# Kernel tuning notes

Measured on AMD Instinct MI355X. Metric: run time of the kernel, lower is better.

Reference implementation:

```python
import jax, jax.numpy as jnp
import numpy as np

IN_DIM = 768
N_HEADS = 12
HEAD_DIM = IN_DIM // N_HEADS


def setup_inputs() -> dict:
    key = jax.random.key(0)
    k1, k2, k3, k4, k5 = jax.random.split(key, 5)
    x = jax.random.normal(k1, (2, 2048, IN_DIM), dtype=jnp.float32)
    s = 1.0 / np.sqrt(IN_DIM)
    W_qkv = jax.random.uniform(k2, (IN_DIM, 3 * IN_DIM), jnp.float32, -s, s)
    b_qkv = jax.random.uniform(k3, (3 * IN_DIM,), jnp.float32, -s, s)
    W_out = jax.random.uniform(k4, (IN_DIM, IN_DIM), jnp.float32, -s, s)
    b_out = jax.random.uniform(k5, (IN_DIM,), jnp.float32, -s, s)
    return {"x": x, "W_qkv": W_qkv, "b_qkv": b_qkv, "W_out": W_out, "b_out": b_out}


def reference(x, W_qkv, b_qkv, W_out, b_out):
    B, N, D = x.shape
    qkv = x @ W_qkv + b_qkv  # [B, N, 3D]
    qkv = qkv.reshape(B, N, 3, N_HEADS, HEAD_DIM)
    qkv = jnp.transpose(qkv, (2, 0, 3, 1, 4))  # [3, B, H, N, Dh]
    q, k, v = qkv[0], qkv[1], qkv[2]
    scale = 1.0 / np.sqrt(HEAD_DIM)
    scores = jnp.einsum("bhqd,bhkd->bhqk", q, k) * scale  # [B, H, N, N]
    attn = jax.nn.softmax(scores, axis=-1)
    out = jnp.einsum("bhqk,bhkd->bhqd", attn, v)  # [B, H, N, Dh]
    out = jnp.transpose(out, (0, 2, 1, 3)).reshape(B, N, D)
    return out @ W_out + b_out
```

## Files before the change

kernel.cpp:

```cpp
#include <hip/hip_runtime.h>

#define DEVI __device__ __forceinline__

typedef __attribute__((ext_vector_type(8))) short short8;
typedef __attribute__((ext_vector_type(4))) float f32x4;
typedef __attribute__((ext_vector_type(16))) float f32x16;

DEVI unsigned short f32_to_bf16(float f) {
  unsigned int u = __float_as_uint(f);
  u += 0x7fffu + ((u >> 16) & 1u);
  return (unsigned short)(u >> 16);
}
DEVI float bf16_to_f32(unsigned short h) {
  return __uint_as_float(((unsigned int)h) << 16);
}

DEVI void gld_lds16(const void* g, void* l) {
  __builtin_amdgcn_global_load_lds(
      (__attribute__((address_space(1))) void*)(g),
      (__attribute__((address_space(3))) void*)(l), 16, 0, 0);
}

__global__ void k_cast_bf16(const float* __restrict__ in, unsigned short* __restrict__ out,
                            int total8) {
  int i = blockIdx.x * blockDim.x + threadIdx.x;
  if (i >= total8) return;
  const float* src = in + i * 8;
  short8 v;
#pragma unroll
  for (int j = 0; j < 8; ++j) v[j] = (short)f32_to_bf16(src[j]);
  *(short8*)&out[(size_t)i * 8] = v;
}

__global__ __launch_bounds__(256) void k_cast_Bt(const float* __restrict__ W,
                                                 unsigned short* __restrict__ Wt,
                                                 int K, int N) {
  int kt = blockIdx.x, nt = blockIdx.y;
  __shared__ float t[32][33];
  int tid = threadIdx.x;
#pragma unroll
  for (int p = 0; p < 4; ++p) {
    int idx = tid + p * 256;
    int rr = idx >> 5, cc = idx & 31;
    t[rr][cc] = W[(size_t)(kt * 32 + rr) * N + nt * 32 + cc];
  }
  __syncthreads();
#pragma unroll
  for (int p = 0; p < 4; ++p) {
    int idx = tid + p * 256;
    int rn = idx >> 5, ck = idx & 31;
    Wt[(size_t)(nt * 32 + rn) * K + kt * 32 + ck] = f32_to_bf16(t[ck][rn]);
  }
}

__global__ __launch_bounds__(256) void k_gemm_qkv(const unsigned short* __restrict__ A,
                                                  const unsigned short* __restrict__ Bt,
                                                  const float* __restrict__ bias,
                                                  int M, int N, int K,
                                                  unsigned short* __restrict__ Qo,
                                                  unsigned short* __restrict__ Ko,
                                                  unsigned short* __restrict__ Vo) {
  __shared__ __align__(16) unsigned short As[128 * 32];
  __shared__ __align__(16) unsigned short Bs[128 * 32];
  int tid = threadIdx.x;
  int tm = blockIdx.x, tn = blockIdx.y;
  int lane = tid & 63, wid = tid >> 6;
  int wr = wid >> 1, wc = wid & 1;
  int g = lane >> 4, lr = lane & 15;
  f32x4 acc[4][4] = {};
  int srow = tid >> 2;
  int scol = (tid & 3) * 8;
  const unsigned short* Ab = A + (size_t)tm * 128 * K;
  const unsigned short* Bb = Bt + (size_t)tn * 128 * K;
  for (int k0 = 0; k0 < K; k0 += 32) {
    gld_lds16(Ab + (size_t)srow * K + k0 + scol, &As[srow * 32 + scol]);
    gld_lds16(Ab + (size_t)(srow + 64) * K + k0 + scol, &As[(srow + 64) * 32 + scol]);
    gld_lds16(Bb + (size_t)srow * K + k0 + scol, &Bs[srow * 32 + scol]);
    gld_lds16(Bb + (size_t)(srow + 64) * K + k0 + scol, &Bs[(srow + 64) * 32 + scol]);
    __syncthreads();
    short8 a[4], b[4];
#pragma unroll
    for (int m = 0; m < 4; ++m)
      a[m] = *(const short8*)&As[(wr * 64 + m * 16 + lr) * 32 + g * 8];
#pragma unroll
    for (int n = 0; n < 4; ++n)
      b[n] = *(const short8*)&Bs[(wc * 64 + n * 16 + lr) * 32 + g * 8];
#pragma unroll
    for (int m = 0; m < 4; ++m)
#pragma unroll
      for (int n = 0; n < 4; ++n)
        acc[m][n] = __builtin_amdgcn_mfma_f32_16x16x32_bf16(a[m], b[n], acc[m][n], 0, 0, 0);
    __syncthreads();
  }
  const float QSCALE = 0.125f * 1.4426950408889634f;
#pragma unroll
  for (int m = 0; m < 4; ++m) {
#pragma unroll
    for (int n = 0; n < 4; ++n) {
      int col = tn * 128 + wc * 64 + n * 16 + lr;
      float bv = bias[col];
      int sec = (col >= 1536) ? 2 : ((col >= 768) ? 1 : 0);
      int c = col - sec * 768;
      int hh = c >> 6, d = c & 63;
#pragma unroll
      for (int j = 0; j < 4; ++j) {
        int row = tm * 128 + wr * 64 + m * 16 + g * 4 + j;
        int bb = row >> 11, nn = row & 2047;
        size_t dst = (((size_t)(bb * 12 + hh) << 11) + nn) * 64 + d;
        float outv = acc[m][n][j] + bv;
        if (sec == 0) {
          Qo[dst] = f32_to_bf16(outv * QSCALE);
        } else if (sec == 1) {
          Ko[dst] = f32_to_bf16(outv);
        } else {
          Vo[dst] = f32_to_bf16(outv);
        }
      }
    }
  }
}

__global__ __launch_bounds__(256) void k_gemm2(const unsigned short* __restrict__ A,
                                               const unsigned short* __restrict__ Bt,
                                               const float* __restrict__ bias,
                                               float* __restrict__ C,
                                               int M, int N, int K) {
  __shared__ __align__(16) unsigned short As[64 * 32];
  __shared__ __align__(16) unsigned short Bs[64 * 32];
  int tid = threadIdx.x;
  int tm = blockIdx.x, tn = blockIdx.y;
  int lane = tid & 63, wid = tid >> 6;
  int wr = wid >> 1, wc = wid & 1;
  int g = lane >> 4, lr = lane & 15;
  f32x4 acc[2][2] = {};
  int srow = tid >> 2;
  int scol = (tid & 3) * 8;
  const unsigned short* Ab = A + (size_t)tm * 64 * K;
  const unsigned short* Bb = Bt + (size_t)tn * 64 * K;
  for (int k0 = 0; k0 < K; k0 += 32) {
    gld_lds16(Ab + (size_t)srow * K + k0 + scol, &As[srow * 32 + scol]);
    gld_lds16(Bb + (size_t)srow * K + k0 + scol, &Bs[srow * 32 + scol]);
    __syncthreads();
    short8 a[2], b[2];
#pragma unroll
    for (int m = 0; m < 2; ++m)
      a[m] = *(const short8*)&As[(wr * 32 + m * 16 + lr) * 32 + g * 8];
#pragma unroll
    for (int n = 0; n < 2; ++n)
      b[n] = *(const short8*)&Bs[(wc * 32 + n * 16 + lr) * 32 + g * 8];
#pragma unroll
    for (int m = 0; m < 2; ++m)
#pragma unroll
      for (int n = 0; n < 2; ++n)
        acc[m][n] = __builtin_amdgcn_mfma_f32_16x16x32_bf16(a[m], b[n], acc[m][n], 0, 0, 0);
    __syncthreads();
  }
#pragma unroll
  for (int m = 0; m < 2; ++m) {
#pragma unroll
    for (int n = 0; n < 2; ++n) {
      int col = tn * 64 + wc * 32 + n * 16 + lr;
      float bv = bias[col];
#pragma unroll
      for (int j = 0; j < 4; ++j) {
        int row = tm * 64 + wr * 32 + m * 16 + g * 4 + j;
        C[(size_t)row * N + col] = acc[m][n][j] + bv;
      }
    }
  }
}

__global__ __launch_bounds__(256) void k_v_transpose(const unsigned short* __restrict__ Vc,
                                                     unsigned short* __restrict__ Vt) {
  int bh = blockIdx.x;
  int nt = blockIdx.y;
  __shared__ unsigned short s[64][65];
  int tid = threadIdx.x;
  int r = tid >> 2;
#pragma unroll
  for (int p = 0; p < 2; ++p) {
    int c = (tid & 3) + p * 4;
    short8 v = *(const short8*)&Vc[((size_t)(bh * 2048 + nt * 64 + r)) * 64 + c * 8];
#pragma unroll
    for (int ii = 0; ii < 8; ++ii) s[r][c * 8 + ii] = (unsigned short)v[ii];
  }
  __syncthreads();
  int d = tid >> 2;
#pragma unroll
  for (int p = 0; p < 2; ++p) {
    int c = (tid & 3) + p * 4;
    short8 w;
#pragma unroll
    for (int ii = 0; ii < 8; ++ii) w[ii] = (short)s[c * 8 + ii][d];
    *(short8*)&Vt[((size_t)bh * 64 + d) * 2048 + nt * 64 + c * 8] = w;
  }
}


#define ATTN_STAGE(KSB, VSB, T)                                                          \
  {                                                                                      \
    int kv0 = (T) * 64;                                                                  \
    _Pragma("unroll") for (int it = 0; it < 4; ++it) {                                   \
      int L = tid + it * 128;                                                            \
      int rw = L >> 3, s7 = L & 7;                                                       \
      gld_lds16(Kb + (size_t)(khead + kv0 + rw) * 64 + ((s7 ^ (rw & 7)) * 8),            \
                &KSB[L * 8]);                                                            \
      gld_lds16(Vt + (size_t)(vhead + rw) * 2048 + kv0 + ((s7 ^ (rw & 7)) * 8),          \
                &VSB[L * 8]);                                                            \
    }                                                                                    \
  }

#define BUILD_PA(S, KS0)                                                                 \
  {                                                                                      \
    unsigned int b0, a0, e0, c0;                                                         \
    asm("v_cvt_pk_bf16_f32 %0, %1, %2" : "=v"(b0) : "v"(S[0]), "v"(S[1]));               \
    asm("v_cvt_pk_bf16_f32 %0, %1, %2" : "=v"(a0) : "v"(S[4]), "v"(S[5]));               \
    asm("v_permlane32_swap_b32 %0, %1" : "+v"(b0), "+v"(a0));                            \
    asm("v_cvt_pk_bf16_f32 %0, %1, %2" : "=v"(e0) : "v"(S[2]), "v"(S[3]));               \
    asm("v_cvt_pk_bf16_f32 %0, %1, %2" : "=v"(c0) : "v"(S[6]), "v"(S[7]));               \
    asm("v_permlane32_swap_b32 %0, %1" : "+v"(e0), "+v"(c0));                            \
    paw[KS0][0] = b0; paw[KS0][1] = e0; paw[KS0][2] = a0; paw[KS0][3] = c0;              \
    unsigned int b1, a1, e1, c1;                                                         \
    asm("v_cvt_pk_bf16_f32 %0, %1, %2" : "=v"(b1) : "v"(S[8]), "v"(S[9]));               \
    asm("v_cvt_pk_bf16_f32 %0, %1, %2" : "=v"(a1) : "v"(S[12]), "v"(S[13]));             \
    asm("v_permlane32_swap_b32 %0, %1" : "+v"(b1), "+v"(a1));                            \
    asm("v_cvt_pk_bf16_f32 %0, %1, %2" : "=v"(e1) : "v"(S[10]), "v"(S[11]));             \
    asm("v_cvt_pk_bf16_f32 %0, %1, %2" : "=v"(c1) : "v"(S[14]), "v"(S[15]));             \
    asm("v_permlane32_swap_b32 %0, %1" : "+v"(e1), "+v"(c1));                            \
    paw[KS0 + 1][0] = b1; paw[KS0 + 1][1] = e1; paw[KS0 + 1][2] = a1; paw[KS0 + 1][3] = c1; \
  }

#define PROC_TILE(KSB, VSB)                                                              \
  {                                                                                      \
    f32x16 sa = {}, sb = {};                                                             \
    __builtin_amdgcn_s_setprio(1);                                                       \
    _Pragma("unroll") for (int ds = 0; ds < 4; ++ds) {                                   \
      short8 kf0 = *(const short8*)&KSB[ln31 * 64 + (((ds * 2 + hi) ^ ln7) * 8)];        \
      short8 kf1 = *(const short8*)&KSB[(32 + ln31) * 64 + (((ds * 2 + hi) ^ ln7) * 8)]; \
      sa = __builtin_amdgcn_mfma_f32_32x32x16_bf16(kf0, qf[ds], sa, 0, 0, 0);            \
      sb = __builtin_amdgcn_mfma_f32_32x32x16_bf16(kf1, qf[ds], sb, 0, 0, 0);            \
    }                                                                                    \
    __builtin_amdgcn_s_setprio(0);                                                       \
    _Pragma("unroll") for (int i = 0; i < 16; ++i) {                                     \
      float pv = exp2f(sa[i]);                                                           \
      sa[i] = pv;                                                                        \
      lrun += pv;                                                                        \
    }                                                                                    \
    _Pragma("unroll") for (int i = 0; i < 16; ++i) {                                     \
      float pv = exp2f(sb[i]);                                                           \
      sb[i] = pv;                                                                        \
      lrun += pv;                                                                        \
    }                                                                                    \
    unsigned int paw[4][4];                                                              \
    BUILD_PA(sa, 0)                                                                      \
    BUILD_PA(sb, 2)                                                                      \
    __builtin_amdgcn_s_setprio(1);                                                       \
    _Pragma("unroll") for (int ks = 0; ks < 4; ++ks) {                                   \
      union {                                                                            \
        unsigned int u[4];                                                               \
        short8 s8;                                                                       \
      } pu;                                                                              \
      pu.u[0] = paw[ks][0];                                                              \
      pu.u[1] = paw[ks][1];                                                              \
      pu.u[2] = paw[ks][2];                                                              \
      pu.u[3] = paw[ks][3];                                                              \
      short8 vb0 = *(const short8*)&VSB[ln31 * 64 + (((ks * 2 + hi) ^ ln7) * 8)];        \
      short8 vb1 = *(const short8*)&VSB[(32 + ln31) * 64 + (((ks * 2 + hi) ^ ln7) * 8)]; \
      oacc0 = __builtin_amdgcn_mfma_f32_32x32x16_bf16(pu.s8, vb0, oacc0, 0, 0, 0);       \
      oacc1 = __builtin_amdgcn_mfma_f32_32x32x16_bf16(pu.s8, vb1, oacc1, 0, 0, 0);       \
    }                                                                                    \
    __builtin_amdgcn_s_setprio(0);                                                       \
  }

__global__ __launch_bounds__(128, 3) void k_attn(const unsigned short* __restrict__ Qb,
                                                 const unsigned short* __restrict__ Kb,
                                                 const unsigned short* __restrict__ Vt,
                                                 unsigned short* __restrict__ Xh) {
  int bh = blockIdx.x;
  int qb = blockIdx.y;
  int b = bh / 12, h = bh - b * 12;
  __shared__ __align__(16) unsigned short Ks0[64 * 64], Ks1[64 * 64];
  __shared__ __align__(16) unsigned short Vs0[64 * 64], Vs1[64 * 64];
  int tid = threadIdx.x;
  int wid = tid >> 6, lane = tid & 63;
  int ln31 = lane & 31, hi = lane >> 5, ln7 = lane & 7;
  int khead = bh * 2048;
  int vhead = bh * 64;
  int q0 = qb * 64 + wid * 32;

  short8 qf[4];
#pragma unroll
  for (int ds = 0; ds < 4; ++ds)
    qf[ds] = *(const short8*)&Qb[(size_t)(khead + q0 + ln31) * 64 + ds * 16 + hi * 8];

  float lrun = 0.f;
  f32x16 oacc0 = {}, oacc1 = {};

  ATTN_STAGE(Ks0, Vs0, 0);
  __syncthreads();
#pragma unroll 1
  for (int tt = 0; tt < 16; ++tt) {
    ATTN_STAGE(Ks1, Vs1, 2 * tt + 1);
    PROC_TILE(Ks0, Vs0);
    __syncthreads();
    if (tt < 15) ATTN_STAGE(Ks0, Vs0, 2 * tt + 2);
    PROC_TILE(Ks1, Vs1);
    __syncthreads();
  }

  lrun += __shfl_xor(lrun, 32, 64);
  float linv = 1.0f / lrun;
#pragma unroll
  for (int r = 0; r < 16; ++r) {
    int qrow = (r & 3) + 8 * (r >> 2) + 4 * hi;
    float lf = __shfl(linv, qrow, 64);
    int grow = b * 2048 + q0 + qrow;
    int colb = h * 64 + ln31;
    Xh[(size_t)grow * 768 + colb] = f32_to_bf16(oacc0[r] * lf);
    Xh[(size_t)grow * 768 + colb + 32] = f32_to_bf16(oacc1[r] * lf);
  }
}

extern "C" void kernel_launch(void* const* d_in, const int* in_sizes, int n_in,
                              void* d_out, int out_size, void* d_ws, size_t ws_size,
                              hipStream_t stream) {
  const float* x = (const float*)d_in[0];
  const float* W_qkv = (const float*)d_in[1];
  const float* b_qkv = (const float*)d_in[2];
  const float* W_out = (const float*)d_in[3];
  const float* b_out = (const float*)d_in[4];
  float* out = (float*)d_out;
  char* ws = (char*)d_ws;

  unsigned short* Xh = (unsigned short*)(ws + 0);
  unsigned short* Xb = (unsigned short*)(ws + 18874368);
  unsigned short* Wq_t = (unsigned short*)(ws + 25165824);
  unsigned short* Wo_t = (unsigned short*)(ws + 28704768);
  unsigned short* Qb = (unsigned short*)(ws + 32243712);
  unsigned short* Kb = (unsigned short*)(ws + 38535168);
  unsigned short* Vc = (unsigned short*)(ws + 44826624);
  unsigned short* Vt = (unsigned short*)(ws + 51118080);

  k_cast_bf16<<<(4096 * 768 / 8 + 255) / 256, 256, 0, stream>>>(x, Xb, 4096 * 768 / 8);
  k_cast_Bt<<<dim3(24, 72), 256, 0, stream>>>(W_qkv, Wq_t, 768, 2304);
  k_cast_Bt<<<dim3(24, 24), 256, 0, stream>>>(W_out, Wo_t, 768, 768);
  k_gemm_qkv<<<dim3(32, 18), 256, 0, stream>>>(Xb, Wq_t, b_qkv, 4096, 2304, 768, Qb, Kb, Vc);
  k_v_transpose<<<dim3(24, 32), 256, 0, stream>>>(Vc, Vt);
  k_attn<<<dim3(24, 32), 128, 0, stream>>>(Qb, Kb, Vt, Xh);
  k_gemm2<<<dim3(64, 12), 256, 0, stream>>>(Xh, Wo_t, b_out, out, 4096, 768, 768);
}
```

Before: 118.2 us.

## Split KV tiles across wave pairs in attention with LDS reduction

Attention blocks grow from 2 to 4 waves. Each pair of waves shares one 32-row query slice and splits every 64-key tile into two 32-key halves. At the end the partial outputs and row sums are reduced through LDS before normalising. The aim is more waves per tile and smaller per-wave register use, to raise occupancy and latency hiding. The cost is an extra LDS round trip and a barrier at the end, and each wave does fewer MFMAs per loaded tile.

```diff
diff --git a/kernel.cpp b/kernel.cpp
--- a/kernel.cpp
+++ b/kernel.cpp
@@ -200,8 +200,8 @@
 #define ATTN_STAGE(KSB, VSB, T)                                                          \
   {                                                                                      \
     int kv0 = (T) * 64;                                                                  \
-    _Pragma("unroll") for (int it = 0; it < 4; ++it) {                                   \
-      int L = tid + it * 128;                                                            \
+    _Pragma("unroll") for (int it = 0; it < 2; ++it) {                                   \
+      int L = tid + it * 256;                                                            \
       int rw = L >> 3, s7 = L & 7;                                                       \
       gld_lds16(Kb + (size_t)(khead + kv0 + rw) * 64 + ((s7 ^ (rw & 7)) * 8),            \
                 &KSB[L * 8]);                                                            \
@@ -210,7 +210,7 @@
     }                                                                                    \
   }
 
-#define BUILD_PA(S, KS0)                                                                 \
+#define BUILD_PA(S)                                                                      \
   {                                                                                      \
     unsigned int b0, a0, e0, c0;                                                         \
     asm("v_cvt_pk_bf16_f32 %0, %1, %2" : "=v"(b0) : "v"(S[0]), "v"(S[1]));               \
@@ -219,7 +219,7 @@
     asm("v_cvt_pk_bf16_f32 %0, %1, %2" : "=v"(e0) : "v"(S[2]), "v"(S[3]));               \
     asm("v_cvt_pk_bf16_f32 %0, %1, %2" : "=v"(c0) : "v"(S[6]), "v"(S[7]));               \
     asm("v_permlane32_swap_b32 %0, %1" : "+v"(e0), "+v"(c0));                            \
-    paw[KS0][0] = b0; paw[KS0][1] = e0; paw[KS0][2] = a0; paw[KS0][3] = c0;              \
+    paw[0][0] = b0; paw[0][1] = e0; paw[0][2] = a0; paw[0][3] = c0;                      \
     unsigned int b1, a1, e1, c1;                                                         \
     asm("v_cvt_pk_bf16_f32 %0, %1, %2" : "=v"(b1) : "v"(S[8]), "v"(S[9]));               \
     asm("v_cvt_pk_bf16_f32 %0, %1, %2" : "=v"(a1) : "v"(S[12]), "v"(S[13]));             \
@@ -227,18 +227,16 @@
     asm("v_cvt_pk_bf16_f32 %0, %1, %2" : "=v"(e1) : "v"(S[10]), "v"(S[11]));             \
     asm("v_cvt_pk_bf16_f32 %0, %1, %2" : "=v"(c1) : "v"(S[14]), "v"(S[15]));             \
     asm("v_permlane32_swap_b32 %0, %1" : "+v"(e1), "+v"(c1));                            \
-    paw[KS0 + 1][0] = b1; paw[KS0 + 1][1] = e1; paw[KS0 + 1][2] = a1; paw[KS0 + 1][3] = c1; \
+    paw[1][0] = b1; paw[1][1] = e1; paw[1][2] = a1; paw[1][3] = c1;                      \
   }
 
 #define PROC_TILE(KSB, VSB)                                                              \
   {                                                                                      \
-    f32x16 sa = {}, sb = {};                                                             \
+    f32x16 sa = {};                                                                      \
     __builtin_amdgcn_s_setprio(1);                                                       \
     _Pragma("unroll") for (int ds = 0; ds < 4; ++ds) {                                   \
-      short8 kf0 = *(const short8*)&KSB[ln31 * 64 + (((ds * 2 + hi) ^ ln7) * 8)];        \
-      short8 kf1 = *(const short8*)&KSB[(32 + ln31) * 64 + (((ds * 2 + hi) ^ ln7) * 8)]; \
-      sa = __builtin_amdgcn_mfma_f32_32x32x16_bf16(kf0, qf[ds], sa, 0, 0, 0);            \
-      sb = __builtin_amdgcn_mfma_f32_32x32x16_bf16(kf1, qf[ds], sb, 0, 0, 0);            \
+      short8 kf = *(const short8*)&KSB[(kh * 32 + ln31) * 64 + (((ds * 2 + hi) ^ ln7) * 8)]; \
+      sa = __builtin_amdgcn_mfma_f32_32x32x16_bf16(kf, qf[ds], sa, 0, 0, 0);             \
     }                                                                                    \
     __builtin_amdgcn_s_setprio(0);                                                       \
     _Pragma("unroll") for (int i = 0; i < 16; ++i) {                                     \
@@ -246,47 +244,46 @@
       sa[i] = pv;                                                                        \
       lrun += pv;                                                                        \
     }                                                                                    \
-    _Pragma("unroll") for (int i = 0; i < 16; ++i) {                                     \
-      float pv = exp2f(sb[i]);                                                           \
-      sb[i] = pv;                                                                        \
-      lrun += pv;                                                                        \
-    }                                                                                    \
-    unsigned int paw[4][4];                                                              \
-    BUILD_PA(sa, 0)                                                                      \
-    BUILD_PA(sb, 2)                                                                      \
+    unsigned int paw[2][4];                                                              \
+    BUILD_PA(sa)                                                                         \
     __builtin_amdgcn_s_setprio(1);                                                       \
-    _Pragma("unroll") for (int ks = 0; ks < 4; ++ks) {                                   \
+    _Pragma("unroll") for (int kl = 0; kl < 2; ++kl) {                                   \
       union {                                                                            \
         unsigned int u[4];                                                               \
         short8 s8;                                                                       \
       } pu;                                                                              \
-      pu.u[0] = paw[ks][0];                                                              \
-      pu.u[1] = paw[ks][1];                                                              \
-      pu.u[2] = paw[ks][2];                                                              \
-      pu.u[3] = paw[ks][3];                                                              \
-      short8 vb0 = *(const short8*)&VSB[ln31 * 64 + (((ks * 2 + hi) ^ ln7) * 8)];        \
-      short8 vb1 = *(const short8*)&VSB[(32 + ln31) * 64 + (((ks * 2 + hi) ^ ln7) * 8)]; \
+      pu.u[0] = paw[kl][0];                                                              \
+      pu.u[1] = paw[kl][1];                                                              \
+      pu.u[2] = paw[kl][2];                                                              \
+      pu.u[3] = paw[kl][3];                                                              \
+      int ksg = kh * 2 + kl;                                                             \
+      short8 vb0 = *(const short8*)&VSB[ln31 * 64 + (((ksg * 2 + hi) ^ ln7) * 8)];       \
+      short8 vb1 = *(const short8*)&VSB[(32 + ln31) * 64 + (((ksg * 2 + hi) ^ ln7) * 8)]; \
       oacc0 = __builtin_amdgcn_mfma_f32_32x32x16_bf16(pu.s8, vb0, oacc0, 0, 0, 0);       \
       oacc1 = __builtin_amdgcn_mfma_f32_32x32x16_bf16(pu.s8, vb1, oacc1, 0, 0, 0);       \
     }                                                                                    \
     __builtin_amdgcn_s_setprio(0);                                                       \
   }
 
-__global__ __launch_bounds__(128, 3) void k_attn(const unsigned short* __restrict__ Qb,
+__global__ __launch_bounds__(256, 4) void k_attn(const unsigned short* __restrict__ Qb,
                                                  const unsigned short* __restrict__ Kb,
                                                  const unsigned short* __restrict__ Vt,
                                                  unsigned short* __restrict__ Xh) {
   int bh = blockIdx.x;
   int qb = blockIdx.y;
   int b = bh / 12, h = bh - b * 12;
-  __shared__ __align__(16) unsigned short Ks0[64 * 64], Ks1[64 * 64];
-  __shared__ __align__(16) unsigned short Vs0[64 * 64], Vs1[64 * 64];
+  __shared__ __align__(16) unsigned short LDSbuf[4 * 64 * 64];
+  unsigned short* Ks0 = LDSbuf;
+  unsigned short* Vs0 = LDSbuf + 64 * 64;
+  unsigned short* Ks1 = LDSbuf + 2 * 64 * 64;
+  unsigned short* Vs1 = LDSbuf + 3 * 64 * 64;
   int tid = threadIdx.x;
   int wid = tid >> 6, lane = tid & 63;
+  int qh = wid >> 1, kh = wid & 1;
   int ln31 = lane & 31, hi = lane >> 5, ln7 = lane & 7;
   int khead = bh * 2048;
   int vhead = bh * 64;
-  int q0 = qb * 64 + wid * 32;
+  int q0 = qb * 64 + qh * 32;
 
   short8 qf[4];
 #pragma unroll
@@ -309,15 +306,36 @@
   }
 
   lrun += __shfl_xor(lrun, 32, 64);
-  float linv = 1.0f / lrun;
-#pragma unroll
-  for (int r = 0; r < 16; ++r) {
-    int qrow = (r & 3) + 8 * (r >> 2) + 4 * hi;
-    float lf = __shfl(linv, qrow, 64);
-    int grow = b * 2048 + q0 + qrow;
-    int colb = h * 64 + ln31;
-    Xh[(size_t)grow * 768 + colb] = f32_to_bf16(oacc0[r] * lf);
-    Xh[(size_t)grow * 768 + colb + 32] = f32_to_bf16(oacc1[r] * lf);
+
+  float* scr = (float*)LDSbuf;
+  if (kh == 1) {
+    float* p = scr + (size_t)(qh * 64 + lane) * 33;
+#pragma unroll
+    for (int i = 0; i < 16; ++i) {
+      p[i] = oacc0[i];
+      p[16 + i] = oacc1[i];
+    }
+    p[32] = lrun;
+  }
+  __syncthreads();
+  if (kh == 0) {
+    float* p = scr + (size_t)(qh * 64 + lane) * 33;
+#pragma unroll
+    for (int i = 0; i < 16; ++i) {
+      oacc0[i] += p[i];
+      oacc1[i] += p[16 + i];
+    }
+    lrun += p[32];
+    float linv = 1.0f / lrun;
+#pragma unroll
+    for (int r = 0; r < 16; ++r) {
+      int qrow = (r & 3) + 8 * (r >> 2) + 4 * hi;
+      float lf = __shfl(linv, qrow, 64);
+      int grow = b * 2048 + q0 + qrow;
+      int colb = h * 64 + ln31;
+      Xh[(size_t)grow * 768 + colb] = f32_to_bf16(oacc0[r] * lf);
+      Xh[(size_t)grow * 768 + colb + 32] = f32_to_bf16(oacc1[r] * lf);
+    }
   }
 }
 
@@ -346,6 +364,6 @@
   k_cast_Bt<<<dim3(24, 24), 256, 0, stream>>>(W_out, Wo_t, 768, 768);
   k_gemm_qkv<<<dim3(32, 18), 256, 0, stream>>>(Xb, Wq_t, b_qkv, 4096, 2304, 768, Qb, Kb, Vc);
   k_v_transpose<<<dim3(24, 32), 256, 0, stream>>>(Vc, Vt);
-  k_attn<<<dim3(24, 32), 128, 0, stream>>>(Qb, Kb, Vt, Xh);
+  k_attn<<<dim3(24, 32), 256, 0, stream>>>(Qb, Kb, Vt, Xh);
   k_gemm2<<<dim3(64, 12), 256, 0, stream>>>(Xh, Wo_t, b_out, out, 4096, 768, 768);
 }
```

New measurement: 105.9 us. 1.12x faster.
